# Optimization experiments

Measured on AMD Instinct MI355X. Metric: run time of the kernel, lower is better.

Reference implementation:

```python
import jax, jax.numpy as jnp
import numpy as np

HID, H, P = 1024, 16, 50  # hid_dim, n_heads, max_relative_position
DH = HID // H


def _rel_idx(len_q, len_k):
    # [Lq, Lk] clipped relative-distance indices into the (2P+1)-row table
    d = jnp.arange(len_k)[None, :] - jnp.arange(len_q)[:, None]
    return jnp.clip(d, -P, P) + P


def setup_inputs() -> dict:
    key = jax.random.key(0)
    ks = jax.random.split(key, 13)
    L, B = 2048, 2
    s = 0.02
    return {
        "query": jax.random.normal(ks[0], (L, B, HID), jnp.float32),
        "key": jax.random.normal(ks[1], (L, B, HID), jnp.float32),
        "value": jax.random.normal(ks[2], (L, B, HID), jnp.float32),
        "Wq": jax.random.normal(ks[3], (HID, HID), jnp.float32) * s,
        "bq": jax.random.normal(ks[4], (HID,), jnp.float32) * s,
        "Wk": jax.random.normal(ks[5], (HID, HID), jnp.float32) * s,
        "bk": jax.random.normal(ks[6], (HID,), jnp.float32) * s,
        "Wv": jax.random.normal(ks[7], (HID, HID), jnp.float32) * s,
        "bv": jax.random.normal(ks[8], (HID,), jnp.float32) * s,
        "Wo": jax.random.normal(ks[9], (HID, HID), jnp.float32) * s,
        "bo": jax.random.normal(ks[10], (HID,), jnp.float32) * s,
        "rel_k": jax.random.normal(ks[11], (2 * P + 1, DH), jnp.float32) * s,
        "rel_v": jax.random.normal(ks[12], (2 * P + 1, DH), jnp.float32) * s,
    }


def reference(query, key, value, Wq, bq, Wk, bk, Wv, bv, Wo, bo, rel_k, rel_v):
    # inputs are seq-first [L, B, hid]; torch code transposes to batch-first
    q = jnp.swapaxes(query, 0, 1)  # [B, Lq, hid]
    k = jnp.swapaxes(key, 0, 1)
    v = jnp.swapaxes(value, 0, 1)
    B, Lq, _ = q.shape
    Lk = k.shape[1]

    q = q @ Wq.T + bq
    k = k @ Wk.T + bk
    v = v @ Wv.T + bv

    # split heads: [B, H, L, DH]
    qh = q.reshape(B, Lq, H, DH).transpose(0, 2, 1, 3)
    kh = k.reshape(B, Lk, H, DH).transpose(0, 2, 1, 3)
    vh = v.reshape(B, Lk, H, DH).transpose(0, 2, 1, 3)

    idx = _rel_idx(Lq, Lk)
    Rk = rel_k[idx]  # [Lq, Lk, DH]
    Rv = rel_v[idx]  # [Lq, Lk, DH]

    attn1 = jnp.einsum('bhqd,bhkd->bhqk', qh, kh)
    attn2 = jnp.einsum('bhqd,qkd->bhqk', qh, Rk)
    scale = jnp.asarray(np.sqrt(DH), qh.dtype)
    attn = jax.nn.softmax((attn1 + attn2) / scale, axis=-1)  # dropout p=0 -> identity

    w1 = jnp.einsum('bhqk,bhkd->bhqd', attn, vh)
    w2 = jnp.einsum('bhqk,qkd->bhqd', attn, Rv)
    x = (w1 + w2).transpose(0, 2, 1, 3).reshape(B, Lq, HID)
    x = x @ Wo.T + bo
    return jnp.swapaxes(x, 0, 1)  # [Lq, B, hid]
```

## Files before the change

### kernel.cpp

```cpp
#include <hip/hip_runtime.h>


#define LSEQ 2048
#define HIDDIM 1024
#define NH 16
#define DHD 64
#define NREL 101
#define PMAX 50
#define SCL 0.18033688011112042f

typedef __attribute__((ext_vector_type(8))) __bf16 bf16x8;
typedef __attribute__((ext_vector_type(4))) float f32x4;

#define MFMA(A, B, C) __builtin_amdgcn_mfma_f32_16x16x32_bf16(A, B, C, 0, 0, 0)
#define LDS_FENCE() asm volatile("s_waitcnt lgkmcnt(0)" ::: "memory")

__device__ __forceinline__ unsigned short f2bf(float f) {
  unsigned int u = __builtin_bit_cast(unsigned int, f);
  u += 0x7fffu + ((u >> 16) & 1u);
  return (unsigned short)(u >> 16);
}
__device__ __forceinline__ float bflo(unsigned int u) { return __builtin_bit_cast(float, u << 16); }

__device__ __forceinline__ unsigned cvtpk(float lo, float hi) {
  unsigned r;
  asm("v_cvt_pk_bf16_f32 %0, %1, %2" : "=v"(r) : "v"(lo), "v"(hi));
  return r;
}
__device__ __forceinline__ float pklo(unsigned pk) { return __builtin_bit_cast(float, pk << 16); }
__device__ __forceinline__ float pkhi(unsigned pk) { return __builtin_bit_cast(float, pk & 0xffff0000u); }

__device__ __forceinline__ uint4 pack8(float4 f0, float4 f1) {
  uint4 o;
  o.x = (unsigned)f2bf(f0.x) | ((unsigned)f2bf(f0.y) << 16);
  o.y = (unsigned)f2bf(f0.z) | ((unsigned)f2bf(f0.w) << 16);
  o.z = (unsigned)f2bf(f1.x) | ((unsigned)f2bf(f1.y) << 16);
  o.w = (unsigned)f2bf(f1.z) | ((unsigned)f2bf(f1.w) << 16);
  return o;
}

__device__ __forceinline__ void gload16(const unsigned short* g, unsigned short* l) {
  __builtin_amdgcn_global_load_lds(
      (const __attribute__((address_space(1))) unsigned int*)g,
      (__attribute__((address_space(3))) unsigned int*)l, 16, 0, 0);
}

__global__ void cast_w4(const float* __restrict__ s0, const float* __restrict__ s1,
                        const float* __restrict__ s2, const float* __restrict__ s3,
                        unsigned short* __restrict__ dst) {
  const int e = (blockIdx.x * 256 + threadIdx.x) * 8;
  const int g = e >> 20;
  const float* s = (g == 0) ? s0 : (g == 1) ? s1 : (g == 2) ? s2 : s3;
  const int o = e & 0xFFFFF;
  const float4 f0 = *(const float4*)(s + o);
  const float4 f1 = *(const float4*)(s + o + 4);
  *(uint4*)(dst + e) = pack8(f0, f1);
}

__global__ void cast_x3(const float* __restrict__ q, const float* __restrict__ k,
                        const float* __restrict__ v,
                        unsigned short* __restrict__ dq, unsigned short* __restrict__ dk,
                        unsigned short* __restrict__ dv) {
  const int gid = blockIdx.x * 256 + threadIdx.x;
  const int segi = gid >> 19;
  const int e = (gid & 0x7FFFF) * 8;
  const float* s = (segi == 0) ? q : (segi == 1) ? k : v;
  unsigned short* dst = (segi == 0) ? dq : (segi == 1) ? dk : dv;
  const int m = e >> 10, kk = e & 1023;
  const int b = m >> 11, l = m & 2047;
  const float* sp = s + (size_t)((l << 1) + b) * HIDDIM + kk;
  const float4 f0 = *(const float4*)sp;
  const float4 f1 = *(const float4*)(sp + 4);
  *(uint4*)(dst + e) = pack8(f0, f1);
}

__global__ void cast_rk_kernel(const float* __restrict__ src, unsigned short* __restrict__ dst) {
  const int e = blockIdx.x * 256 + threadIdx.x;
  if (e >= 112 * 64) return;
  dst[e] = (e < NREL * 64) ? f2bf(src[e]) : (unsigned short)0;
}

__global__ void cast_rv_kernel(const float* __restrict__ src, unsigned short* __restrict__ dst) {
  const int e = blockIdx.x * 256 + threadIdx.x;
  if (e >= 64 * 128) return;
  const int d = e >> 7, j = e & 127;
  dst[e] = (j < NREL) ? f2bf(src[j * DHD + d]) : (unsigned short)0;
}

__global__ __launch_bounds__(256, 3) void gemm_qkv(
    const unsigned short* __restrict__ Xq, const unsigned short* __restrict__ Xk,
    const unsigned short* __restrict__ Xv, const unsigned short* __restrict__ Wcat,
    const float* __restrict__ bq, const float* __restrict__ bk, const float* __restrict__ bv,
    unsigned short* __restrict__ Qb, unsigned short* __restrict__ Kb,
    unsigned short* __restrict__ Vgt) {
  __shared__ __align__(16) unsigned short SH[17408];
  unsigned short* LA = SH;
  unsigned short* LB = SH + 8192;

  const int tid = threadIdx.x;
  const int seg = blockIdx.x >> 8;
  const int t = blockIdx.x & 255;
  const int m0 = (t >> 3) * 128, n0 = (t & 7) * 128;

  const unsigned short* A = (seg == 0) ? Xq : (seg == 1) ? Xk : Xv;
  const unsigned short* W = Wcat + ((size_t)seg << 20);
  const float* bias = (seg == 0) ? bq : (seg == 1) ? bk : bv;

  const int lane = tid & 63, w = tid >> 6;
  const int c = lane & 15, quad = lane >> 4;

  const int srow = w * 32 + (lane >> 3);
  const int scol = ((lane & 7) ^ (lane >> 3)) << 3;
  const unsigned short* pA = A + (size_t)(m0 + srow) * 1024 + scol;
  const unsigned short* pW = W + (size_t)(n0 + srow) * 1024 + scol;
  unsigned short* lA = LA + w * 2048;
  unsigned short* lB = LB + w * 2048;

  const int wr = w >> 1, wc = w & 1;
  const int cx = (c & 7) << 3;

  f32x4 acc[4][4] = {};

  for (int k0 = 0; k0 < 1024; k0 += 64) {
#pragma unroll
    for (int i = 0; i < 4; i++) {
      gload16(pA + k0 + i * 8192, lA + i * 512);
      gload16(pW + k0 + i * 8192, lB + i * 512);
    }
    __syncthreads();
#pragma unroll
    for (int ks = 0; ks < 2; ks++) {
      bf16x8 af[4], bfr[4];
#pragma unroll
      for (int f = 0; f < 4; f++) {
        af[f]  = *(const bf16x8*)&LA[(wr * 64 + f * 16 + c) * 64 + ((ks * 32 + quad * 8) ^ cx)];
        bfr[f] = *(const bf16x8*)&LB[(wc * 64 + f * 16 + c) * 64 + ((ks * 32 + quad * 8) ^ cx)];
      }
#pragma unroll
      for (int i = 0; i < 4; i++)
#pragma unroll
        for (int j = 0; j < 4; j++)
          acc[i][j] = MFMA(af[i], bfr[j], acc[i][j]);
    }
    __syncthreads();
  }

  const int b = m0 >> 11, l0 = m0 & 2047;
  const int h0 = n0 >> 6;
  if (seg < 2) {
    unsigned short* out = seg ? Kb : Qb;
#pragma unroll
    for (int i = 0; i < 4; i++)
#pragma unroll
      for (int j = 0; j < 4; j++) {
        const int nl = wc * 64 + j * 16 + c;
        const float bv_ = bias[n0 + nl];
        const int h = h0 + (nl >> 6), d = nl & 63;
#pragma unroll
        for (int r = 0; r < 4; r++) {
          const int l = l0 + wr * 64 + i * 16 + quad * 4 + r;
          out[((size_t)((b * NH + h) * LSEQ + l) << 6) + d] = f2bf(acc[i][j][r] + bv_);
        }
      }
  } else {
    unsigned short* Ct = SH;
#pragma unroll
    for (int i = 0; i < 4; i++)
#pragma unroll
      for (int j = 0; j < 4; j++) {
        const int nl = wc * 64 + j * 16 + c;
        const float bv_ = bias[n0 + nl];
#pragma unroll
        for (int r = 0; r < 4; r++) {
          const int ml = wr * 64 + i * 16 + quad * 4 + r;
          Ct[nl * 136 + ml] = f2bf(acc[i][j][r] + bv_);
        }
      }
    __syncthreads();
    const int dr = tid >> 1, lc = (tid & 1) * 64;
    const int h = h0 + (dr >> 6), dd = dr & 63;
    unsigned short* dst = Vgt + ((size_t)((b * NH + h) * 64 + dd)) * LSEQ + l0 + lc;
    const unsigned short* src = Ct + dr * 136 + lc;
#pragma unroll
    for (int u = 0; u < 8; u++)
      *(uint4*)(dst + u * 8) = *(const uint4*)(src + u * 8);
  }
}

template <int MODE>
__global__ __launch_bounds__(256, 4) void gemm64(
    const unsigned short* __restrict__ A,
    const unsigned short* __restrict__ W,
    const float* __restrict__ bias,
    float* __restrict__ outF,
    unsigned short* __restrict__ outB) {
  constexpr int K = 1024;
  __shared__ unsigned short As[64 * 72];
  __shared__ unsigned short Bs[64 * 72];
  const int tid = threadIdx.x;
  const int tm = blockIdx.x >> 4, tn = blockIdx.x & 15;
  const int m0 = tm * 64, n0 = tn * 64;
  const int lane = tid & 63, wave = tid >> 6;
  const int wm = (wave >> 1) * 32, wn = (wave & 1) * 32;
  const int qr = lane & 15, quad = lane >> 4;
  const int sr = tid >> 3, sc = (tid & 7) * 8;
  f32x4 acc[2][2] = {};
  for (int k0 = 0; k0 < K; k0 += 64) {
    *(uint4*)&As[sr * 72 + sc]        = *(const uint4*)&A[(size_t)(m0 + sr) * K + k0 + sc];
    *(uint4*)&As[(sr + 32) * 72 + sc] = *(const uint4*)&A[(size_t)(m0 + sr + 32) * K + k0 + sc];
    *(uint4*)&Bs[sr * 72 + sc]        = *(const uint4*)&W[(size_t)(n0 + sr) * K + k0 + sc];
    *(uint4*)&Bs[(sr + 32) * 72 + sc] = *(const uint4*)&W[(size_t)(n0 + sr + 32) * K + k0 + sc];
    __syncthreads();
#pragma unroll
    for (int ks = 0; ks < 64; ks += 32) {
      bf16x8 a0 = *(const bf16x8*)&As[(wm + qr) * 72 + ks + quad * 8];
      bf16x8 a1 = *(const bf16x8*)&As[(wm + 16 + qr) * 72 + ks + quad * 8];
      bf16x8 b0 = *(const bf16x8*)&Bs[(wn + qr) * 72 + ks + quad * 8];
      bf16x8 b1 = *(const bf16x8*)&Bs[(wn + 16 + qr) * 72 + ks + quad * 8];
      acc[0][0] = MFMA(a0, b0, acc[0][0]);
      acc[0][1] = MFMA(a0, b1, acc[0][1]);
      acc[1][0] = MFMA(a1, b0, acc[1][0]);
      acc[1][1] = MFMA(a1, b1, acc[1][1]);
    }
    __syncthreads();
  }
#pragma unroll
  for (int i = 0; i < 2; i++)
#pragma unroll
    for (int j = 0; j < 2; j++) {
      const int n = n0 + wn + 16 * j + qr;
      const float bv = bias[n];
#pragma unroll
      for (int rr = 0; rr < 4; rr++) {
        const int m = m0 + wm + 16 * i + quad * 4 + rr;
        const float v = acc[i][j][rr] + bv;
        const int b = m >> 11, l = m & 2047;
        if (MODE == 1) {
          outF[(size_t)((l << 1) + b) * HIDDIM + n] = v;
        }
      }
    }
}

#define KT 32
__global__ __launch_bounds__(256, 4) void attn_mfma(
    const unsigned short* __restrict__ Qb,
    const unsigned short* __restrict__ Kb,
    const unsigned short* __restrict__ Vgt,
    const unsigned short* __restrict__ RKb,
    const unsigned short* __restrict__ RVb,
    unsigned short* __restrict__ outB) {
  __shared__ __align__(16) unsigned short SH[20480];
  unsigned short* Kst = SH;

  const int tid = threadIdx.x;
  const int xcd = blockIdx.x & 7, slot = blockIdx.x >> 3;
  const int bh = (slot >> 5) * 8 + xcd;
  const int q0 = (slot & 31) * 64;

  const int lane = tid & 63, wq = tid >> 6;
  const int c = lane & 15, quad = lane >> 4;
  unsigned short* Ptw = SH + 4608 + wq * 640;
  unsigned short* Tb  = SH + 7168 + wq * 1664;
  unsigned short* SrS = SH + 13824 + wq * 1664;

  const size_t base = (size_t)bh * (LSEQ * DHD);
  const unsigned short* Qp = Qb + base;
  const unsigned short* Kp = Kb + base;
  const unsigned short* Vp = Vgt + base;

  const int qrow_w = q0 + wq * 16;

  {
    uint4 z = {0u, 0u, 0u, 0u};
    uint4* tz = (uint4*)(SH + 7168);
    for (int e = tid; e < 832; e += 256) tz[e] = z;
  }

  const bf16x8 aq0 = *(const bf16x8*)&Qp[(size_t)(qrow_w + c) * DHD + quad * 8];
  const bf16x8 aq1 = *(const bf16x8*)&Qp[(size_t)(qrow_w + c) * DHD + 32 + quad * 8];

#pragma unroll
  for (int jt = 0; jt < 7; jt++) {
    const bf16x8 rk0 = *(const bf16x8*)&RKb[(jt * 16 + c) * DHD + quad * 8];
    const bf16x8 rk1 = *(const bf16x8*)&RKb[(jt * 16 + c) * DHD + 32 + quad * 8];
    f32x4 s4 = {};
    s4 = MFMA(rk0, aq0, s4);
    s4 = MFMA(rk1, aq1, s4);
    const int jb = jt * 16 + quad * 4;
    const unsigned p01 = cvtpk(s4[0], s4[1]);
    const unsigned p23 = cvtpk(s4[2], s4[3]);
    if (jb <= 102)     *(unsigned*)&SrS[c * 104 + jb] = p01;
    if (jb + 2 <= 102) *(unsigned*)&SrS[c * 104 + jb + 2] = p23;
  }

  const int strow = tid >> 3, stcol = (tid & 7) * 8;
  {
    uint4 k0r = *(const uint4*)&Kp[(size_t)strow * DHD + stcol];
    *(uint4*)&Kst[strow * 72 + stcol] = k0r;
  }
  __syncthreads();

  const float srvlo = bflo((unsigned)SrS[c * 104 + 0]);
  const float srvhi = bflo((unsigned)SrS[c * 104 + 100]);

  float lows = 0.f, highs = 0.f, mids = 0.f;
  f32x4 Od[4] = {};

  for (int it = 0; it < 64; ++it) {
    const int k0 = it * KT;
    const int cur = (it & 1) * 2304;
    uint4 kreg;
    if (it < 63) kreg = *(const uint4*)&Kp[(size_t)(k0 + KT + strow) * DHD + stcol];
    bf16x8 vf[4];
#pragma unroll
    for (int t = 0; t < 4; t++)
      vf[t] = *(const bf16x8*)&Vp[(size_t)(t * 16 + c) * LSEQ + k0 + quad * 8];

    const bf16x8 ka00 = *(const bf16x8*)&Kst[cur + c * 72 + quad * 8];
    const bf16x8 ka01 = *(const bf16x8*)&Kst[cur + c * 72 + 32 + quad * 8];
    const bf16x8 ka10 = *(const bf16x8*)&Kst[cur + (16 + c) * 72 + quad * 8];
    const bf16x8 ka11 = *(const bf16x8*)&Kst[cur + (16 + c) * 72 + 32 + quad * 8];
    f32x4 s0 = {}, s1 = {};
    s0 = MFMA(ka00, aq0, s0);
    s0 = MFMA(ka01, aq1, s0);
    s1 = MFMA(ka10, aq0, s1);
    s1 = MFMA(ka11, aq1, s1);

    const int mode = (k0 + KT - 1 <= qrow_w - 50) ? 0 : (k0 >= qrow_w + 65) ? 2 : 1;

    unsigned pkA0, pkA1, pkB0, pkB1;
    if (mode != 1) {
      const float srv = (mode == 0) ? srvlo : srvhi;
      const float e0 = exp2f((s0[0] + srv) * SCL);
      const float e1 = exp2f((s0[1] + srv) * SCL);
      const float e2 = exp2f((s0[2] + srv) * SCL);
      const float e3 = exp2f((s0[3] + srv) * SCL);
      const float e4 = exp2f((s1[0] + srv) * SCL);
      const float e5 = exp2f((s1[1] + srv) * SCL);
      const float e6 = exp2f((s1[2] + srv) * SCL);
      const float e7 = exp2f((s1[3] + srv) * SCL);
      pkA0 = cvtpk(e0, e1); pkA1 = cvtpk(e2, e3);
      pkB0 = cvtpk(e4, e5); pkB1 = cvtpk(e6, e7);
      const float sq = ((pklo(pkA0) + pkhi(pkA0)) + (pklo(pkA1) + pkhi(pkA1)))
                     + ((pklo(pkB0) + pkhi(pkB0)) + (pklo(pkB1) + pkhi(pkB1)));
      if (mode == 0) lows += sq; else highs += sq;
    } else {
      const int kb0 = k0 + quad * 4 - (qrow_w + c) + 50;
      float ee[8]; int jj[8];
#pragma unroll
      for (int r = 0; r < 4; r++) {
        int j0 = kb0 + r;       j0 = j0 < 0 ? 0 : (j0 > 100 ? 100 : j0);
        int j1 = kb0 + 16 + r;  j1 = j1 < 0 ? 0 : (j1 > 100 ? 100 : j1);
        jj[r] = j0; jj[4 + r] = j1;
        const float sv0 = bflo((unsigned)SrS[c * 104 + j0]);
        const float sv1 = bflo((unsigned)SrS[c * 104 + j1]);
        ee[r]     = exp2f((s0[r] + sv0) * SCL);
        ee[4 + r] = exp2f((s1[r] + sv1) * SCL);
      }
      pkA0 = cvtpk(ee[0], ee[1]); pkA1 = cvtpk(ee[2], ee[3]);
      pkB0 = cvtpk(ee[4], ee[5]); pkB1 = cvtpk(ee[6], ee[7]);
      const unsigned pks[4] = {pkA0, pkA1, pkB0, pkB1};
#pragma unroll
      for (int i = 0; i < 4; i++) {
        const unsigned pk = pks[i];
        const float plo = pklo(pk), phi = pkhi(pk);
        const int jl = jj[2 * i], jh = jj[2 * i + 1];
        if (jl == 0) lows += plo;
        else if (jl == 100) highs += plo;
        else { mids += plo; Tb[c * 104 + jl] = (unsigned short)pk; }
        if (jh == 0) lows += phi;
        else if (jh == 100) highs += phi;
        else { mids += phi; Tb[c * 104 + jh] = (unsigned short)(pk >> 16); }
      }
    }

    uint2 w0; w0.x = pkA0; w0.y = pkA1;
    uint2 w1; w1.x = pkB0; w1.y = pkB1;
    *(uint2*)&Ptw[c * 40 + quad * 4] = w0;
    *(uint2*)&Ptw[c * 40 + 16 + quad * 4] = w1;
    LDS_FENCE();
    const bf16x8 ap = *(const bf16x8*)&Ptw[c * 40 + quad * 8];
#pragma unroll
    for (int t = 0; t < 4; t++)
      Od[t] = MFMA(ap, vf[t], Od[t]);

    if (it < 63) *(uint4*)&Kst[(cur ^ 2304) + strow * 72 + stcol] = kreg;
    __syncthreads();
  }

#pragma unroll
  for (int m = 16; m < 64; m <<= 1) {
    lows  += __shfl_xor(lows,  m, 64);
    highs += __shfl_xor(highs, m, 64);
    mids  += __shfl_xor(mids,  m, 64);
  }
  const float rsum = (lows + highs) + mids;
  if (lane < 16) {
    Tb[c * 104 + 0]   = f2bf(lows);
    Tb[c * 104 + 100] = f2bf(highs);
  }
  LDS_FENCE();

#pragma unroll
  for (int kc = 0; kc < 4; kc++) {
    uint4 zz = {0u, 0u, 0u, 0u};
    bf16x8 at = __builtin_bit_cast(bf16x8, zz);
    if (kc < 3 || quad == 0) at = *(const bf16x8*)&Tb[c * 104 + kc * 32 + quad * 8];
#pragma unroll
    for (int t = 0; t < 4; t++) {
      const bf16x8 bv = *(const bf16x8*)&RVb[(t * 16 + c) * 128 + kc * 32 + quad * 8];
      Od[t] = MFMA(at, bv, Od[t]);
    }
  }

  const int b = bh >> 4, h = bh & 15;
#pragma unroll
  for (int r = 0; r < 4; r++) {
    const float rs = __shfl(rsum, quad * 4 + r, 64);
    const float inv = 1.f / rs;
    const int qg = qrow_w + quad * 4 + r;
    unsigned short* op = outB + (size_t)(b * LSEQ + qg) * HIDDIM + h * DHD + c;
#pragma unroll
    for (int t = 0; t < 4; t++) op[t * 16] = f2bf(Od[t][r] * inv);
  }
}

extern "C" void kernel_launch(void* const* d_in, const int* in_sizes, int n_in,
                              void* d_out, int out_size, void* d_ws, size_t ws_size,
                              hipStream_t stream) {
  const float* query = (const float*)d_in[0];
  const float* key   = (const float*)d_in[1];
  const float* value = (const float*)d_in[2];
  const float* Wq = (const float*)d_in[3];  const float* bq = (const float*)d_in[4];
  const float* Wk = (const float*)d_in[5];  const float* bk = (const float*)d_in[6];
  const float* Wv = (const float*)d_in[7];  const float* bv = (const float*)d_in[8];
  const float* Wo = (const float*)d_in[9];  const float* bo = (const float*)d_in[10];
  const float* relk = (const float*)d_in[11];
  const float* relv = (const float*)d_in[12];
  float* out = (float*)d_out;

  char* w = (char*)d_ws;
  const size_t MB = 1ull << 20;
  unsigned short* Wcat = (unsigned short*)(w + 0 * MB);
  unsigned short* Wob  = (unsigned short*)(w + 6 * MB);
  unsigned short* Xq   = (unsigned short*)(w + 8 * MB);
  unsigned short* Qb   = (unsigned short*)(w + 16 * MB);
  unsigned short* Kb   = (unsigned short*)(w + 24 * MB);
  unsigned short* Vgt  = (unsigned short*)(w + 32 * MB);
  unsigned short* AOb  = Xq;
  unsigned short* RKb  = Wcat;
  unsigned short* RVb  = (unsigned short*)(w + 2 * MB);
  unsigned short* Xk = (unsigned short*)out;
  unsigned short* Xv = (unsigned short*)out + (4u << 20);

  cast_w4<<<2048, 256, 0, stream>>>(Wq, Wk, Wv, Wo, Wcat);
  cast_x3<<<6144, 256, 0, stream>>>(query, key, value, Xq, Xk, Xv);
  gemm_qkv<<<768, 256, 0, stream>>>(Xq, Xk, Xv, Wcat, bq, bk, bv, Qb, Kb, Vgt);
  cast_rk_kernel<<<28, 256, 0, stream>>>(relk, RKb);
  cast_rv_kernel<<<32, 256, 0, stream>>>(relv, RVb);
  attn_mfma<<<1024, 256, 0, stream>>>(Qb, Kb, Vgt, RKb, RVb, AOb);
  gemm64<1><<<1024, 256, 0, stream>>>(AOb, Wob, bo, out, nullptr);
}
```

Measured before the change: 335.8 us.

## Load K fragments directly from global, drop LDS K staging and block barriers

Each wave now reads its K fragments straight from global memory into registers instead of staging K tiles in a shared double buffer. This removes the per-iteration __syncthreads and the cross-wave LDS traffic, so waves can run independently. The smaller LDS footprint allows raising launch bounds to 5 blocks per CU, and the LDS fence gains a sched_barrier to keep ordering. The cost is redundant global/L2 reads of K, since all four waves now fetch the same tile, and higher load latency exposed per iteration.

```diff
diff --git a/kernel.cpp b/kernel.cpp
--- a/kernel.cpp
+++ b/kernel.cpp
@@ -13,7 +13,10 @@
 typedef __attribute__((ext_vector_type(4))) float f32x4;
 
 #define MFMA(A, B, C) __builtin_amdgcn_mfma_f32_16x16x32_bf16(A, B, C, 0, 0, 0)
-#define LDS_FENCE() asm volatile("s_waitcnt lgkmcnt(0)" ::: "memory")
+#define LDS_FENCE() do { \
+    asm volatile("s_waitcnt lgkmcnt(0)" ::: "memory"); \
+    __builtin_amdgcn_sched_barrier(0); \
+  } while (0)
 
 __device__ __forceinline__ unsigned short f2bf(float f) {
   unsigned int u = __builtin_bit_cast(unsigned int, f);
@@ -243,15 +246,14 @@
 }
 
 #define KT 32
-__global__ __launch_bounds__(256, 4) void attn_mfma(
+__global__ __launch_bounds__(256, 5) void attn_mfma(
     const unsigned short* __restrict__ Qb,
     const unsigned short* __restrict__ Kb,
     const unsigned short* __restrict__ Vgt,
     const unsigned short* __restrict__ RKb,
     const unsigned short* __restrict__ RVb,
     unsigned short* __restrict__ outB) {
-  __shared__ __align__(16) unsigned short SH[20480];
-  unsigned short* Kst = SH;
+  __shared__ __align__(16) unsigned short SH[15872];
 
   const int tid = threadIdx.x;
   const int xcd = blockIdx.x & 7, slot = blockIdx.x >> 3;
@@ -260,9 +262,9 @@
 
   const int lane = tid & 63, wq = tid >> 6;
   const int c = lane & 15, quad = lane >> 4;
-  unsigned short* Ptw = SH + 4608 + wq * 640;
-  unsigned short* Tb  = SH + 7168 + wq * 1664;
-  unsigned short* SrS = SH + 13824 + wq * 1664;
+  unsigned short* Ptw = SH + wq * 640;
+  unsigned short* Tb  = SH + 2560 + wq * 1664;
+  unsigned short* SrS = SH + 9216 + wq * 1664;
 
   const size_t base = (size_t)bh * (LSEQ * DHD);
   const unsigned short* Qp = Qb + base;
@@ -273,8 +275,10 @@
 
   {
     uint4 z = {0u, 0u, 0u, 0u};
-    uint4* tz = (uint4*)(SH + 7168);
-    for (int e = tid; e < 832; e += 256) tz[e] = z;
+    uint4* tz = (uint4*)Tb;
+#pragma unroll
+    for (int i = 0; i < 3; i++) tz[lane + 64 * i] = z;
+    if (lane < 16) tz[lane + 192] = z;
   }
 
   const bf16x8 aq0 = *(const bf16x8*)&Qp[(size_t)(qrow_w + c) * DHD + quad * 8];
@@ -293,13 +297,7 @@
     if (jb <= 102)     *(unsigned*)&SrS[c * 104 + jb] = p01;
     if (jb + 2 <= 102) *(unsigned*)&SrS[c * 104 + jb + 2] = p23;
   }
-
-  const int strow = tid >> 3, stcol = (tid & 7) * 8;
-  {
-    uint4 k0r = *(const uint4*)&Kp[(size_t)strow * DHD + stcol];
-    *(uint4*)&Kst[strow * 72 + stcol] = k0r;
-  }
-  __syncthreads();
+  LDS_FENCE();
 
   const float srvlo = bflo((unsigned)SrS[c * 104 + 0]);
   const float srvhi = bflo((unsigned)SrS[c * 104 + 100]);
@@ -309,18 +307,15 @@
 
   for (int it = 0; it < 64; ++it) {
     const int k0 = it * KT;
-    const int cur = (it & 1) * 2304;
-    uint4 kreg;
-    if (it < 63) kreg = *(const uint4*)&Kp[(size_t)(k0 + KT + strow) * DHD + stcol];
+    const bf16x8 ka00 = *(const bf16x8*)&Kp[(size_t)(k0 + c) * DHD + quad * 8];
+    const bf16x8 ka01 = *(const bf16x8*)&Kp[(size_t)(k0 + c) * DHD + 32 + quad * 8];
+    const bf16x8 ka10 = *(const bf16x8*)&Kp[(size_t)(k0 + 16 + c) * DHD + quad * 8];
+    const bf16x8 ka11 = *(const bf16x8*)&Kp[(size_t)(k0 + 16 + c) * DHD + 32 + quad * 8];
     bf16x8 vf[4];
 #pragma unroll
     for (int t = 0; t < 4; t++)
       vf[t] = *(const bf16x8*)&Vp[(size_t)(t * 16 + c) * LSEQ + k0 + quad * 8];
 
-    const bf16x8 ka00 = *(const bf16x8*)&Kst[cur + c * 72 + quad * 8];
-    const bf16x8 ka01 = *(const bf16x8*)&Kst[cur + c * 72 + 32 + quad * 8];
-    const bf16x8 ka10 = *(const bf16x8*)&Kst[cur + (16 + c) * 72 + quad * 8];
-    const bf16x8 ka11 = *(const bf16x8*)&Kst[cur + (16 + c) * 72 + 32 + quad * 8];
     f32x4 s0 = {}, s1 = {};
     s0 = MFMA(ka00, aq0, s0);
     s0 = MFMA(ka01, aq1, s0);
@@ -384,9 +379,6 @@
 #pragma unroll
     for (int t = 0; t < 4; t++)
       Od[t] = MFMA(ap, vf[t], Od[t]);
-
-    if (it < 63) *(uint4*)&Kst[(cur ^ 2304) + strow * 72 + stcol] = kreg;
-    __syncthreads();
   }
 
 #pragma unroll
```

Result: slower. 428.2 us (+27.5%).

## Retile output projection to 128x128 with swizzled direct-to-LDS loads; merge rel casts

Applied to the files above, without the earlier changes.

Replaces the 64x64-tile output GEMM with a 128x128-tile kernel modeled on the QKV GEMM. It uses gload16 direct global-to-LDS copies, an XOR-swizzled LDS layout and a 4x4 MFMA accumulator per wave, which raises arithmetic intensity and cuts redundant global loads. It also merges the two small relative-table cast kernels into one launch. The trade-off is fewer blocks (256) and higher register pressure per wave.

```diff
diff --git a/kernel.cpp b/kernel.cpp
--- a/kernel.cpp
+++ b/kernel.cpp
@@ -74,17 +74,17 @@
   *(uint4*)(dst + e) = pack8(f0, f1);
 }
 
-__global__ void cast_rk_kernel(const float* __restrict__ src, unsigned short* __restrict__ dst) {
+__global__ void cast_rel(const float* __restrict__ rk, const float* __restrict__ rv,
+                         unsigned short* __restrict__ dk, unsigned short* __restrict__ dv) {
   const int e = blockIdx.x * 256 + threadIdx.x;
-  if (e >= 112 * 64) return;
-  dst[e] = (e < NREL * 64) ? f2bf(src[e]) : (unsigned short)0;
-}
-
-__global__ void cast_rv_kernel(const float* __restrict__ src, unsigned short* __restrict__ dst) {
-  const int e = blockIdx.x * 256 + threadIdx.x;
-  if (e >= 64 * 128) return;
-  const int d = e >> 7, j = e & 127;
-  dst[e] = (j < NREL) ? f2bf(src[j * DHD + d]) : (unsigned short)0;
+  if (e < 112 * 64) {
+    dk[e] = (e < NREL * 64) ? f2bf(rk[e]) : (unsigned short)0;
+  } else {
+    const int e2 = e - 112 * 64;
+    if (e2 >= 64 * 128) return;
+    const int d = e2 >> 7, j = e2 & 127;
+    dv[e2] = (j < NREL) ? f2bf(rv[j * DHD + d]) : (unsigned short)0;
+  }
 }
 
 __global__ __launch_bounds__(256, 3) void gemm_qkv(
@@ -187,57 +187,69 @@
   }
 }
 
-template <int MODE>
-__global__ __launch_bounds__(256, 4) void gemm64(
+__global__ __launch_bounds__(256, 3) void gemm_out(
     const unsigned short* __restrict__ A,
     const unsigned short* __restrict__ W,
     const float* __restrict__ bias,
-    float* __restrict__ outF,
-    unsigned short* __restrict__ outB) {
-  constexpr int K = 1024;
-  __shared__ unsigned short As[64 * 72];
-  __shared__ unsigned short Bs[64 * 72];
+    float* __restrict__ outF) {
+  __shared__ __align__(16) unsigned short SH[16384];
+  unsigned short* LA = SH;
+  unsigned short* LB = SH + 8192;
+
   const int tid = threadIdx.x;
-  const int tm = blockIdx.x >> 4, tn = blockIdx.x & 15;
-  const int m0 = tm * 64, n0 = tn * 64;
-  const int lane = tid & 63, wave = tid >> 6;
-  const int wm = (wave >> 1) * 32, wn = (wave & 1) * 32;
-  const int qr = lane & 15, quad = lane >> 4;
-  const int sr = tid >> 3, sc = (tid & 7) * 8;
-  f32x4 acc[2][2] = {};
-  for (int k0 = 0; k0 < K; k0 += 64) {
-    *(uint4*)&As[sr * 72 + sc]        = *(const uint4*)&A[(size_t)(m0 + sr) * K + k0 + sc];
-    *(uint4*)&As[(sr + 32) * 72 + sc] = *(const uint4*)&A[(size_t)(m0 + sr + 32) * K + k0 + sc];
-    *(uint4*)&Bs[sr * 72 + sc]        = *(const uint4*)&W[(size_t)(n0 + sr) * K + k0 + sc];
-    *(uint4*)&Bs[(sr + 32) * 72 + sc] = *(const uint4*)&W[(size_t)(n0 + sr + 32) * K + k0 + sc];
-    __syncthreads();
-#pragma unroll
-    for (int ks = 0; ks < 64; ks += 32) {
-      bf16x8 a0 = *(const bf16x8*)&As[(wm + qr) * 72 + ks + quad * 8];
-      bf16x8 a1 = *(const bf16x8*)&As[(wm + 16 + qr) * 72 + ks + quad * 8];
-      bf16x8 b0 = *(const bf16x8*)&Bs[(wn + qr) * 72 + ks + quad * 8];
-      bf16x8 b1 = *(const bf16x8*)&Bs[(wn + 16 + qr) * 72 + ks + quad * 8];
-      acc[0][0] = MFMA(a0, b0, acc[0][0]);
-      acc[0][1] = MFMA(a0, b1, acc[0][1]);
-      acc[1][0] = MFMA(a1, b0, acc[1][0]);
-      acc[1][1] = MFMA(a1, b1, acc[1][1]);
-    }
-    __syncthreads();
-  }
-#pragma unroll
-  for (int i = 0; i < 2; i++)
-#pragma unroll
-    for (int j = 0; j < 2; j++) {
-      const int n = n0 + wn + 16 * j + qr;
-      const float bv = bias[n];
-#pragma unroll
-      for (int rr = 0; rr < 4; rr++) {
-        const int m = m0 + wm + 16 * i + quad * 4 + rr;
-        const float v = acc[i][j][rr] + bv;
-        const int b = m >> 11, l = m & 2047;
-        if (MODE == 1) {
-          outF[(size_t)((l << 1) + b) * HIDDIM + n] = v;
-        }
+  const int t = blockIdx.x;
+  const int m0 = (t >> 3) * 128, n0 = (t & 7) * 128;
+
+  const int lane = tid & 63, w = tid >> 6;
+  const int c = lane & 15, quad = lane >> 4;
+
+  const int srow = w * 32 + (lane >> 3);
+  const int scol = ((lane & 7) ^ (lane >> 3)) << 3;
+  const unsigned short* pA = A + (size_t)(m0 + srow) * 1024 + scol;
+  const unsigned short* pW = W + (size_t)(n0 + srow) * 1024 + scol;
+  unsigned short* lA = LA + w * 2048;
+  unsigned short* lB = LB + w * 2048;
+
+  const int wr = w >> 1, wc = w & 1;
+  const int cx = (c & 7) << 3;
+
+  f32x4 acc[4][4] = {};
+
+  for (int k0 = 0; k0 < 1024; k0 += 64) {
+#pragma unroll
+    for (int i = 0; i < 4; i++) {
+      gload16(pA + k0 + i * 8192, lA + i * 512);
+      gload16(pW + k0 + i * 8192, lB + i * 512);
+    }
+    __syncthreads();
+#pragma unroll
+    for (int ks = 0; ks < 2; ks++) {
+      bf16x8 af[4], bfr[4];
+#pragma unroll
+      for (int f = 0; f < 4; f++) {
+        af[f]  = *(const bf16x8*)&LA[(wr * 64 + f * 16 + c) * 64 + ((ks * 32 + quad * 8) ^ cx)];
+        bfr[f] = *(const bf16x8*)&LB[(wc * 64 + f * 16 + c) * 64 + ((ks * 32 + quad * 8) ^ cx)];
+      }
+#pragma unroll
+      for (int i = 0; i < 4; i++)
+#pragma unroll
+        for (int j = 0; j < 4; j++)
+          acc[i][j] = MFMA(af[i], bfr[j], acc[i][j]);
+    }
+    __syncthreads();
+  }
+
+  const int b = m0 >> 11, l0 = m0 & 2047;
+#pragma unroll
+  for (int i = 0; i < 4; i++)
+#pragma unroll
+    for (int j = 0; j < 4; j++) {
+      const int n = n0 + wc * 64 + j * 16 + c;
+      const float bv_ = bias[n];
+#pragma unroll
+      for (int r = 0; r < 4; r++) {
+        const int l = l0 + wr * 64 + i * 16 + quad * 4 + r;
+        outF[(size_t)((l << 1) + b) * HIDDIM + n] = acc[i][j][r] + bv_;
       }
     }
 }
@@ -457,8 +469,7 @@
   cast_w4<<<2048, 256, 0, stream>>>(Wq, Wk, Wv, Wo, Wcat);
   cast_x3<<<6144, 256, 0, stream>>>(query, key, value, Xq, Xk, Xv);
   gemm_qkv<<<768, 256, 0, stream>>>(Xq, Xk, Xv, Wcat, bq, bk, bv, Qb, Kb, Vgt);
-  cast_rk_kernel<<<28, 256, 0, stream>>>(relk, RKb);
-  cast_rv_kernel<<<32, 256, 0, stream>>>(relv, RVb);
+  cast_rel<<<60, 256, 0, stream>>>(relk, relv, RKb, RVb);
   attn_mfma<<<1024, 256, 0, stream>>>(Qb, Kb, Vgt, RKb, RVb, AOb);
-  gemm64<1><<<1024, 256, 0, stream>>>(AOb, Wob, bo, out, nullptr);
-}
+  gemm_out<<<256, 256, 0, stream>>>(AOb, Wob, bo, out);
+}
```

After: 325.9 us. 2.9% less time.
